# Optimization experiments

Hardware: AMD Instinct MI355X
Metric: run time of the kernel (lower is better)

## Reference

```python
import jax, jax.numpy as jnp
import numpy as np

B, S, D, H = 2, 4096, 1024, 16
DK = D // H


def setup_inputs() -> dict:
    key = jax.random.key(0)
    ks = jax.random.split(key, 8)
    q = jax.random.normal(ks[0], (B, S, D), dtype=jnp.float32)
    k = jax.random.normal(ks[1], (B, S, D), dtype=jnp.float32)
    v = jax.random.normal(ks[2], (B, S, D), dtype=jnp.float32)
    mask = jax.random.randint(ks[3], (1, 1, S, S), 0, 2, dtype=jnp.int32)
    # torch.nn.Linear weights, y = x @ W.T ; Kaiming-uniform-ish init scale
    lim = 1.0 / np.sqrt(D)
    Wq = jax.random.uniform(ks[4], (D, D), jnp.float32, -lim, lim)
    Wk = jax.random.uniform(ks[5], (D, D), jnp.float32, -lim, lim)
    Wv = jax.random.uniform(ks[6], (D, D), jnp.float32, -lim, lim)
    Wo = jax.random.uniform(ks[7], (D, D), jnp.float32, -lim, lim)
    return {"q": q, "k": k, "v": v, "mask": mask,
            "Wq": Wq, "Wk": Wk, "Wv": Wv, "Wo": Wo}


def reference(q, k, v, mask, Wq, Wk, Wv, Wo):
    # Linear projections (torch Linear: x @ W.T), split into heads [B,H,S,DK]
    def heads(x, W):
        return (x @ W.T).reshape(B, S, H, DK).transpose(0, 2, 1, 3)

    Q, K, V = heads(q, Wq), heads(k, Wk), heads(v, Wv)
    scale = 1.0 / jnp.sqrt(jnp.asarray(DK, dtype=Q.dtype))
    # [B,H,S,S] score matrix (original materializes it fully)
    scores = jnp.einsum("bhqd,bhkd->bhqk", Q, K) * scale
    # NOTE: original calls masked_fill without assignment -> mask is a no-op.
    # Dropout: eval-mode identity (original also references missing self.dropout).
    attn = jax.nn.softmax(scores, axis=-1)
    out = jnp.einsum("bhqk,bhkd->bhqd", attn, V)  # [B,H,S,DK]
    out = out.transpose(0, 2, 1, 3).reshape(B, S, D)
    return out @ Wo.T
```

## Files before the change

### kernel.cpp

```cpp
#include <hip/hip_runtime.h>
#include <cstdint>
#include <cstddef>

using u16 = unsigned short;
using u32 = unsigned int;

typedef _Float16 f16x8 __attribute__((ext_vector_type(8)));
typedef float    f32x4 __attribute__((ext_vector_type(4)));
typedef float    f32x16 __attribute__((ext_vector_type(16)));

#define MFMA16(a,b,c) __builtin_amdgcn_mfma_f32_16x16x32_f16((a),(b),(c),0,0,0)
#define MFMA32(a,b,c) __builtin_amdgcn_mfma_f32_32x32x16_f16((a),(b),(c),0,0,0)

__device__ __forceinline__ u16 f2h(float f) {
  return __builtin_bit_cast(u16, (_Float16)f);
}
__device__ __forceinline__ u32 pkrtz(float a, float b) {
  return __builtin_bit_cast(u32, __builtin_amdgcn_cvt_pkrtz(a, b));
}
__device__ __forceinline__ void plswap(u32 &a, u32 &b) {
  asm volatile("v_permlane32_swap_b32 %0, %1" : "+v"(a), "+v"(b));
}
__device__ __forceinline__ void async16(const void* g, void* lds) {
  __builtin_amdgcn_global_load_lds((const __attribute__((address_space(1))) void*)g,
                                   (__attribute__((address_space(3))) void*)lds,
                                   16, 0, 0);
}
#if __has_builtin(__builtin_amdgcn_exp2f)
__device__ __forceinline__ float exp2_hw(float x) { return __builtin_amdgcn_exp2f(x); }
#else
__device__ __forceinline__ float exp2_hw(float x) {
  float r; asm("v_exp_f32 %0, %1" : "=v"(r) : "v"(x)); return r;
}
#endif

__global__ __launch_bounds__(256) void cvt4_w(const float* __restrict__ w0,
                                              const float* __restrict__ w1,
                                              const float* __restrict__ w2,
                                              const float* __restrict__ w3,
                                              u16* __restrict__ d0, u16* __restrict__ d1,
                                              u16* __restrict__ d2, u16* __restrict__ d3,
                                              int n4, float scale0) {
  const int y = blockIdx.y;
  const float* in = y == 0 ? w0 : (y == 1 ? w1 : (y == 2 ? w2 : w3));
  u16* out = y == 0 ? d0 : (y == 1 ? d1 : (y == 2 ? d2 : d3));
  const float sc = y == 0 ? scale0 : 1.0f;
  int i = blockIdx.x * 256 + threadIdx.x;
  const int stride = gridDim.x * 256;
  for (; i < n4; i += stride) {
    const float4 f = reinterpret_cast<const float4*>(in)[i];
    ushort4 o;
    o.x = f2h(f.x * sc); o.y = f2h(f.y * sc);
    o.z = f2h(f.z * sc); o.w = f2h(f.w * sc);
    reinterpret_cast<ushort4*>(out)[i] = o;
  }
}

__global__ __launch_bounds__(256) void cvt3_x(const float* __restrict__ q,
                                              const float* __restrict__ k,
                                              const float* __restrict__ v,
                                              u16* __restrict__ xq, u16* __restrict__ xk,
                                              u16* __restrict__ xv, int n4) {
  const int y = blockIdx.y;
  const float* in = y == 0 ? q : (y == 1 ? k : v);
  u16* out = y == 0 ? xq : (y == 1 ? xk : xv);
  int i = blockIdx.x * 256 + threadIdx.x;
  const int stride = gridDim.x * 256;
  for (; i < n4; i += stride) {
    const float4 f = reinterpret_cast<const float4*>(in)[i];
    ushort4 o;
    o.x = f2h(f.x); o.y = f2h(f.y); o.z = f2h(f.z); o.w = f2h(f.w);
    reinterpret_cast<ushort4*>(out)[i] = o;
  }
}

template <int OF32>
__device__ __forceinline__ void gemm_body(const u16* __restrict__ A,
                                          const u16* __restrict__ Bw,
                                          float* __restrict__ Cf,
                                          u16* __restrict__ Ch,
                                          int M, int N, int K) {
  __shared__ __align__(16) u16 Asm[128 * 64];
  __shared__ __align__(16) u16 Bsm[128 * 64];
  const int tid = threadIdx.x;
  const int w = tid >> 6, l = tid & 63;
  const int wr = w >> 1, wc = w & 1;
  const int m0 = blockIdx.y * 128, n0 = blockIdx.x * 128;
  const int lr = l >> 3, lc = l & 7, csrc = lc ^ lr;
  const int laneq = l & 15, laneg = l >> 4;
  f32x4 acc[4][4] = {};
  for (int k0 = 0; k0 < K; k0 += 64) {
    __syncthreads();
#pragma unroll
    for (int c = 0; c < 4; ++c) {
      const int row = c * 32 + w * 8 + lr;
      async16(A + (size_t)(m0 + row) * K + k0 + csrc * 8, &Asm[c * 2048 + w * 512]);
      async16(Bw + (size_t)(n0 + row) * K + k0 + csrc * 8, &Bsm[c * 2048 + w * 512]);
    }
    __syncthreads();
#pragma unroll
    for (int ks = 0; ks < 2; ++ks) {
      f16x8 af[4], bfr[4];
#pragma unroll
      for (int mi = 0; mi < 4; ++mi) {
        const int row = wr * 64 + mi * 16 + laneq;
        const int ch = (ks * 4 + laneg) ^ (row & 7);
        af[mi] = *(const f16x8*)&Asm[row * 64 + ch * 8];
      }
#pragma unroll
      for (int ni = 0; ni < 4; ++ni) {
        const int row = wc * 64 + ni * 16 + laneq;
        const int ch = (ks * 4 + laneg) ^ (row & 7);
        bfr[ni] = *(const f16x8*)&Bsm[row * 64 + ch * 8];
      }
#pragma unroll
      for (int mi = 0; mi < 4; ++mi)
#pragma unroll
        for (int ni = 0; ni < 4; ++ni)
          acc[mi][ni] = MFMA16(af[mi], bfr[ni], acc[mi][ni]);
    }
  }
#pragma unroll
  for (int mi = 0; mi < 4; ++mi)
#pragma unroll
    for (int r = 0; r < 4; ++r) {
      const int gm = m0 + wr * 64 + mi * 16 + laneg * 4 + r;
#pragma unroll
      for (int ni = 0; ni < 4; ++ni) {
        const int gn = n0 + wc * 64 + ni * 16 + laneq;
        if constexpr (OF32) Cf[(size_t)gm * N + gn] = acc[mi][ni][r];
        else                Ch[(size_t)gm * N + gn] = f2h(acc[mi][ni][r]);
      }
    }
}

__global__ __launch_bounds__(256) void gemm_qk(const u16* __restrict__ xq,
                                               const u16* __restrict__ wq,
                                               u16* __restrict__ Qp,
                                               const u16* __restrict__ xk,
                                               const u16* __restrict__ wk,
                                               u16* __restrict__ Kp) {
  const bool zk = blockIdx.z != 0;
  gemm_body<0>(zk ? xk : xq, zk ? wk : wq, nullptr, zk ? Kp : Qp, 8192, 1024, 1024);
}

__global__ __launch_bounds__(256) void gemm_h(const u16* __restrict__ A,
                                              const u16* __restrict__ Bw,
                                              u16* __restrict__ Ch,
                                              int M, int N, int K) {
  gemm_body<0>(A, Bw, nullptr, Ch, M, N, K);
}

__global__ __launch_bounds__(256) void gemm_f(const u16* __restrict__ A,
                                              const u16* __restrict__ Bw,
                                              float* __restrict__ Cf,
                                              int M, int N, int K) {
  gemm_body<1>(A, Bw, Cf, nullptr, M, N, K);
}

__global__ __launch_bounds__(256, 4) void attn_fwd(const u16* __restrict__ Qp,
                                                   const u16* __restrict__ Kp,
                                                   const u16* __restrict__ VT,
                                                   u16* __restrict__ AO) {
  union SM {
    struct { u16 K[2][64 * 64]; u16 V[2][64 * 64]; } st;
    u16 osm[4][32 * 72];
  };
  __shared__ __align__(16) SM sm;
  const int tid = threadIdx.x, w = tid >> 6, l = tid & 63;
  const int l31 = l & 31, hi = l >> 5, l7 = l & 7, lr = l >> 3;
  const int bid = blockIdx.x;
  const int slot = bid >> 3;
  const int bh = (bid & 7) * 4 + (slot >> 5), qx = slot & 31;
  const int b = bh >> 4, h = bh & 15;
  const int q0 = qx * 128;
  const size_t hb = (size_t)b * 4096 * 1024 + (size_t)h * 64;
  const u16* Kh = Kp + hb;
  const u16* Vh = VT + (size_t)h * 64 * 8192 + (size_t)b * 4096;
  const int csrc = l7 ^ lr;

  f16x8 qf[4];
  {
    const u16* qp = Qp + hb + (size_t)(q0 + w * 32 + l31) * 1024 + hi * 8;
#pragma unroll
    for (int kk = 0; kk < 4; ++kk) qf[kk] = *(const f16x8*)(qp + kk * 16);
  }

  f32x16 zero16;
#pragma unroll
  for (int r = 0; r < 16; ++r) zero16[r] = 0.f;
  f16x8 ones;
#pragma unroll
  for (int r = 0; r < 8; ++r) ones[r] = (_Float16)1.0f;

  f32x16 acc[2];
  f32x16 accl;
#pragma unroll
  for (int r = 0; r < 16; ++r) { acc[0][r] = 0.f; acc[1][r] = 0.f; accl[r] = 0.f; }

  int koff = (w * 8 + lr) * 1024 + csrc * 8;
  int voff = (w * 8 + lr) * 8192 + csrc * 8;

  async16(Kh + koff,             &sm.st.K[0][w * 512]);
  async16(Kh + koff + 32 * 1024, &sm.st.K[0][w * 512 + 2048]);
  async16(Vh + voff,             &sm.st.V[0][w * 512]);
  async16(Vh + voff + 32 * 8192, &sm.st.V[0][w * 512 + 2048]);

  for (int t = 0; t < 64; ++t) {
    const int cur = t & 1;
    __syncthreads();
    if (t < 63) {
      koff += 64 * 1024;
      voff += 64;
      async16(Kh + koff,             &sm.st.K[cur ^ 1][w * 512]);
      async16(Kh + koff + 32 * 1024, &sm.st.K[cur ^ 1][w * 512 + 2048]);
      async16(Vh + voff,             &sm.st.V[cur ^ 1][w * 512]);
      async16(Vh + voff + 32 * 8192, &sm.st.V[cur ^ 1][w * 512 + 2048]);
    }
    const u16* Ks = sm.st.K[cur];
    const u16* Vs = sm.st.V[cur];
#pragma unroll
    for (int kt = 0; kt < 2; ++kt) {
      __builtin_amdgcn_s_setprio(1);
      f16x8 kf = *(const f16x8*)&Ks[(kt * 32 + l31) * 64 + ((hi ^ l7) << 3)];
      f32x16 sv = MFMA32(kf, qf[0], zero16);
#pragma unroll
      for (int kk = 1; kk < 4; ++kk) {
        kf = *(const f16x8*)&Ks[(kt * 32 + l31) * 64 + (((kk * 2 + hi) ^ l7) << 3)];
        sv = MFMA32(kf, qf[kk], sv);
      }
      __builtin_amdgcn_s_setprio(0);
#pragma unroll
      for (int r = 0; r < 16; ++r) sv[r] = exp2_hw(sv[r]);
      f16x8 pf[2];
#pragma unroll
      for (int half = 0; half < 2; ++half) {
        const int rb = half * 8;
        u32 a0 = pkrtz(sv[rb + 0], sv[rb + 1]);
        u32 a1 = pkrtz(sv[rb + 2], sv[rb + 3]);
        u32 b0 = pkrtz(sv[rb + 4], sv[rb + 5]);
        u32 b1 = pkrtz(sv[rb + 6], sv[rb + 7]);
        plswap(a0, b0);
        plswap(a1, b1);
        union { u32 ww[4]; f16x8 v; } uu;
        uu.ww[0] = a0; uu.ww[1] = a1; uu.ww[2] = b0; uu.ww[3] = b1;
        pf[half] = uu.v;
      }
      __builtin_amdgcn_s_setprio(1);
#pragma unroll
      for (int half = 0; half < 2; ++half) {
        accl = MFMA32(ones, pf[half], accl);
#pragma unroll
        for (int ds = 0; ds < 2; ++ds) {
          const f16x8 vf = *(const f16x8*)&Vs[(ds * 32 + l31) * 64 + (((kt * 4 + half * 2 + hi) ^ l7) << 3)];
          acc[ds] = MFMA32(vf, pf[half], acc[ds]);
        }
      }
      __builtin_amdgcn_s_setprio(0);
    }
  }
  __syncthreads();
  {
    const float rn = 1.f / accl[0];
#pragma unroll
    for (int ds = 0; ds < 2; ++ds)
#pragma unroll
      for (int g = 0; g < 4; ++g) {
        uint2 val;
        val.x = pkrtz(acc[ds][4 * g + 0] * rn, acc[ds][4 * g + 1] * rn);
        val.y = pkrtz(acc[ds][4 * g + 2] * rn, acc[ds][4 * g + 3] * rn);
        *(uint2*)&sm.osm[w][l31 * 72 + ds * 32 + g * 8 + hi * 4] = val;
      }
  }
  asm volatile("s_waitcnt lgkmcnt(0)" ::: "memory");
#pragma unroll
  for (int i = 0; i < 4; ++i) {
    const int row = lr + i * 8;
    const uint4 vv = *(const uint4*)&sm.osm[w][row * 72 + l7 * 8];
    *(uint4*)(AO + hb + (size_t)(q0 + w * 32 + row) * 1024 + l7 * 8) = vv;
  }
}

extern "C" void kernel_launch(void* const* d_in, const int* in_sizes, int n_in,
                              void* d_out, int out_size, void* d_ws, size_t ws_size,
                              hipStream_t stream) {
  const float* q  = (const float*)d_in[0];
  const float* k  = (const float*)d_in[1];
  const float* v  = (const float*)d_in[2];
  const float* Wq = (const float*)d_in[4];
  const float* Wk = (const float*)d_in[5];
  const float* Wv = (const float*)d_in[6];
  const float* Wo = (const float*)d_in[7];
  float* out = (float*)d_out;

  char* ws = (char*)d_ws;
  u16* xq  = (u16*)ws;
  u16* xk  = (u16*)(ws + 16777216);
  u16* xv  = (u16*)(ws + 2 * 16777216);
  u16* Qp  = (u16*)(ws + 3 * 16777216);
  u16* Kpp = (u16*)(ws + 4 * 16777216);
  u16* wqb = (u16*)(ws + 5 * 16777216);
  u16* wkb = wqb + 1048576;
  u16* wvb = wkb + 1048576;
  u16* wob = wvb + 1048576;
  u16* VT  = xq;
  u16* AO  = xv;

  constexpr float SC = 0.125f * 1.44269504088896340736f;
  cvt4_w<<<dim3(256, 4), 256, 0, stream>>>(Wq, Wk, Wv, Wo, wqb, wkb, wvb, wob,
                                           262144, SC);
  cvt3_x<<<dim3(1024, 3), 256, 0, stream>>>(q, k, v, xq, xk, xv, 2097152);

  gemm_qk<<<dim3(8, 64, 2), 256, 0, stream>>>(xq, wqb, Qp, xk, wkb, Kpp);
  gemm_h<<<dim3(64, 8), 256, 0, stream>>>(wvb, xv, VT, 1024, 8192, 1024);

  attn_fwd<<<1024, 256, 0, stream>>>(Qp, Kpp, VT, AO);

  gemm_f<<<dim3(8, 64), 256, 0, stream>>>(AO, wob, out, 8192, 1024, 1024);
}
```

Baseline: 284.9 us.

## Merge V projection into QK GEMM launch and software-pipeline attention inner loop

The V projection GEMM is folded into the Q/K projection kernel as a third grid z-slice, which removes one launch and lets all three projections share one wave of blocks. In the attention kernel, the two 32-key sub-tiles are unrolled by hand. The second QK MFMA chain is issued before the first sub-tile's PV MFMAs, with a sched_barrier, so exp and pack work can overlap with matrix instructions. This raises register pressure, which may hurt occupancy at the 4-wave launch bound.

After: 283.6 us. Within noise of the previous version (-0.4%).

```diff
diff --git a/kernel.cpp b/kernel.cpp
--- a/kernel.cpp
+++ b/kernel.cpp
@@ -79,13 +79,12 @@
                                           const u16* __restrict__ Bw,
                                           float* __restrict__ Cf,
                                           u16* __restrict__ Ch,
-                                          int M, int N, int K) {
+                                          int m0, int n0, int N, int K) {
   __shared__ __align__(16) u16 Asm[128 * 64];
   __shared__ __align__(16) u16 Bsm[128 * 64];
   const int tid = threadIdx.x;
   const int w = tid >> 6, l = tid & 63;
   const int wr = w >> 1, wc = w & 1;
-  const int m0 = blockIdx.y * 128, n0 = blockIdx.x * 128;
   const int lr = l >> 3, lc = l & 7, csrc = lc ^ lr;
   const int laneq = l & 15, laneg = l >> 4;
   f32x4 acc[4][4] = {};
@@ -134,28 +133,30 @@
     }
 }
 
-__global__ __launch_bounds__(256) void gemm_qk(const u16* __restrict__ xq,
-                                               const u16* __restrict__ wq,
-                                               u16* __restrict__ Qp,
-                                               const u16* __restrict__ xk,
-                                               const u16* __restrict__ wk,
-                                               u16* __restrict__ Kp) {
-  const bool zk = blockIdx.z != 0;
-  gemm_body<0>(zk ? xk : xq, zk ? wk : wq, nullptr, zk ? Kp : Qp, 8192, 1024, 1024);
-}
-
-__global__ __launch_bounds__(256) void gemm_h(const u16* __restrict__ A,
-                                              const u16* __restrict__ Bw,
-                                              u16* __restrict__ Ch,
-                                              int M, int N, int K) {
-  gemm_body<0>(A, Bw, nullptr, Ch, M, N, K);
+__global__ __launch_bounds__(256) void gemm_qkv(const u16* __restrict__ xq,
+                                                const u16* __restrict__ wq,
+                                                u16* __restrict__ Qp,
+                                                const u16* __restrict__ xk,
+                                                const u16* __restrict__ wk,
+                                                u16* __restrict__ Kp,
+                                                const u16* __restrict__ xv,
+                                                const u16* __restrict__ wv,
+                                                u16* __restrict__ VT) {
+  const int z = blockIdx.z;
+  if (z == 2) {
+    gemm_body<0>(wv, xv, nullptr, VT, blockIdx.x * 128, blockIdx.y * 128, 8192, 1024);
+  } else {
+    const bool zk = z != 0;
+    gemm_body<0>(zk ? xk : xq, zk ? wk : wq, nullptr, zk ? Kp : Qp,
+                 blockIdx.y * 128, blockIdx.x * 128, 1024, 1024);
+  }
 }
 
 __global__ __launch_bounds__(256) void gemm_f(const u16* __restrict__ A,
                                               const u16* __restrict__ Bw,
                                               float* __restrict__ Cf,
-                                              int M, int N, int K) {
-  gemm_body<1>(A, Bw, Cf, nullptr, M, N, K);
+                                              int N, int K) {
+  gemm_body<1>(A, Bw, Cf, nullptr, blockIdx.y * 128, blockIdx.x * 128, N, K);
 }
 
 __global__ __launch_bounds__(256, 4) void attn_fwd(const u16* __restrict__ Qp,
@@ -219,45 +220,83 @@
     }
     const u16* Ks = sm.st.K[cur];
     const u16* Vs = sm.st.V[cur];
-#pragma unroll
-    for (int kt = 0; kt < 2; ++kt) {
-      __builtin_amdgcn_s_setprio(1);
-      f16x8 kf = *(const f16x8*)&Ks[(kt * 32 + l31) * 64 + ((hi ^ l7) << 3)];
-      f32x16 sv = MFMA32(kf, qf[0], zero16);
+
+    __builtin_amdgcn_s_setprio(1);
+    f32x16 sv;
+    {
+      f16x8 kf = *(const f16x8*)&Ks[l31 * 64 + ((hi ^ l7) << 3)];
+      sv = MFMA32(kf, qf[0], zero16);
 #pragma unroll
       for (int kk = 1; kk < 4; ++kk) {
-        kf = *(const f16x8*)&Ks[(kt * 32 + l31) * 64 + (((kk * 2 + hi) ^ l7) << 3)];
+        kf = *(const f16x8*)&Ks[l31 * 64 + (((kk * 2 + hi) ^ l7) << 3)];
         sv = MFMA32(kf, qf[kk], sv);
       }
-      __builtin_amdgcn_s_setprio(0);
-#pragma unroll
-      for (int r = 0; r < 16; ++r) sv[r] = exp2_hw(sv[r]);
-      f16x8 pf[2];
-#pragma unroll
-      for (int half = 0; half < 2; ++half) {
-        const int rb = half * 8;
-        u32 a0 = pkrtz(sv[rb + 0], sv[rb + 1]);
-        u32 a1 = pkrtz(sv[rb + 2], sv[rb + 3]);
-        u32 b0 = pkrtz(sv[rb + 4], sv[rb + 5]);
-        u32 b1 = pkrtz(sv[rb + 6], sv[rb + 7]);
-        plswap(a0, b0);
-        plswap(a1, b1);
-        union { u32 ww[4]; f16x8 v; } uu;
-        uu.ww[0] = a0; uu.ww[1] = a1; uu.ww[2] = b0; uu.ww[3] = b1;
-        pf[half] = uu.v;
-      }
-      __builtin_amdgcn_s_setprio(1);
-#pragma unroll
-      for (int half = 0; half < 2; ++half) {
-        accl = MFMA32(ones, pf[half], accl);
-#pragma unroll
-        for (int ds = 0; ds < 2; ++ds) {
-          const f16x8 vf = *(const f16x8*)&Vs[(ds * 32 + l31) * 64 + (((kt * 4 + half * 2 + hi) ^ l7) << 3)];
-          acc[ds] = MFMA32(vf, pf[half], acc[ds]);
-        }
-      }
-      __builtin_amdgcn_s_setprio(0);
-    }
+    }
+    __builtin_amdgcn_s_setprio(0);
+#pragma unroll
+    for (int r = 0; r < 16; ++r) sv[r] = exp2_hw(sv[r]);
+    f16x8 pf0[2];
+#pragma unroll
+    for (int half = 0; half < 2; ++half) {
+      const int rb = half * 8;
+      u32 a0 = pkrtz(sv[rb + 0], sv[rb + 1]);
+      u32 a1 = pkrtz(sv[rb + 2], sv[rb + 3]);
+      u32 b0 = pkrtz(sv[rb + 4], sv[rb + 5]);
+      u32 b1 = pkrtz(sv[rb + 6], sv[rb + 7]);
+      plswap(a0, b0);
+      plswap(a1, b1);
+      union { u32 ww[4]; f16x8 v; } uu;
+      uu.ww[0] = a0; uu.ww[1] = a1; uu.ww[2] = b0; uu.ww[3] = b1;
+      pf0[half] = uu.v;
+    }
+    __builtin_amdgcn_s_setprio(1);
+    {
+      f16x8 kf = *(const f16x8*)&Ks[(32 + l31) * 64 + ((hi ^ l7) << 3)];
+      sv = MFMA32(kf, qf[0], zero16);
+#pragma unroll
+      for (int kk = 1; kk < 4; ++kk) {
+        kf = *(const f16x8*)&Ks[(32 + l31) * 64 + (((kk * 2 + hi) ^ l7) << 3)];
+        sv = MFMA32(kf, qf[kk], sv);
+      }
+    }
+    __builtin_amdgcn_sched_barrier(0);
+#pragma unroll
+    for (int half = 0; half < 2; ++half) {
+      accl = MFMA32(ones, pf0[half], accl);
+#pragma unroll
+      for (int ds = 0; ds < 2; ++ds) {
+        const f16x8 vf = *(const f16x8*)&Vs[(ds * 32 + l31) * 64 + (((half * 2 + hi) ^ l7) << 3)];
+        acc[ds] = MFMA32(vf, pf0[half], acc[ds]);
+      }
+    }
+    __builtin_amdgcn_s_setprio(0);
+#pragma unroll
+    for (int r = 0; r < 16; ++r) sv[r] = exp2_hw(sv[r]);
+    f16x8 pf1[2];
+#pragma unroll
+    for (int half = 0; half < 2; ++half) {
+      const int rb = half * 8;
+      u32 a0 = pkrtz(sv[rb + 0], sv[rb + 1]);
+      u32 a1 = pkrtz(sv[rb + 2], sv[rb + 3]);
+      u32 b0 = pkrtz(sv[rb + 4], sv[rb + 5]);
+      u32 b1 = pkrtz(sv[rb + 6], sv[rb + 7]);
+      plswap(a0, b0);
+      plswap(a1, b1);
+      union { u32 ww[4]; f16x8 v; } uu;
+      uu.ww[0] = a0; uu.ww[1] = a1; uu.ww[2] = b0; uu.ww[3] = b1;
+      pf1[half] = uu.v;
+    }
+    __builtin_amdgcn_s_setprio(1);
+#pragma unroll
+    for (int half = 0; half < 2; ++half) {
+      accl = MFMA32(ones, pf1[half], accl);
+#pragma unroll
+      for (int ds = 0; ds < 2; ++ds) {
+        const f16x8 vf = *(const f16x8*)&Vs[(ds * 32 + l31) * 64 + (((4 + half * 2 + hi) ^ l7) << 3)];
+        acc[ds] = MFMA32(vf, pf1[half], acc[ds]);
+      }
+    }
+    __builtin_amdgcn_s_setprio(0);
   }
   __syncthreads();
   {
@@ -311,10 +350,10 @@
                                            262144, SC);
   cvt3_x<<<dim3(1024, 3), 256, 0, stream>>>(q, k, v, xq, xk, xv, 2097152);
 
-  gemm_qk<<<dim3(8, 64, 2), 256, 0, stream>>>(xq, wqb, Qp, xk, wkb, Kpp);
-  gemm_h<<<dim3(64, 8), 256, 0, stream>>>(wvb, xv, VT, 1024, 8192, 1024);
+  gemm_qkv<<<dim3(8, 64, 3), 256, 0, stream>>>(xq, wqb, Qp, xk, wkb, Kpp,
+                                               xv, wvb, VT);
 
   attn_fwd<<<1024, 256, 0, stream>>>(Qp, Kpp, VT, AO);
 
-  gemm_f<<<dim3(8, 64), 256, 0, stream>>>(AO, wob, out, 8192, 1024, 1024);
-}
+  gemm_f<<<dim3(8, 64), 256, 0, stream>>>(AO, wob, out, 1024, 1024);
+}
```
